# Performance work log

Hardware: AMD Instinct MI355X
Metric: run time of the kernel (lower is better)

The kernel has to match this reference:

```python
import jax, jax.numpy as jnp
import numpy as np

V, E, H, K = 50000, 256, 256, 16   # vocab, embed_dim, bi_lstm_hidden, n_tags (E must equal H)
HD = H // 2                        # per-direction hidden
B, NSEG, S = 32, 8, 128            # batch, segments, segment size
T = NSEG * S


def _lstm_dir(x, mask, Wih, Whh, b, h0, c0, reverse):
    """Masked (packed-equivalent) unidirectional LSTM. x:[T,B,E], mask:[T,B]."""
    def step(carry, inp):
        h, c = carry
        xt, mt = inp
        g = xt @ Wih.T + h @ Whh.T + b
        i, f, gg, o = jnp.split(g, 4, axis=-1)  # torch gate order i,f,g,o
        cn = jax.nn.sigmoid(f) * c + jax.nn.sigmoid(i) * jnp.tanh(gg)
        hn = jax.nn.sigmoid(o) * jnp.tanh(cn)
        m = mt[:, None]
        return (jnp.where(m, hn, h), jnp.where(m, cn, c)), jnp.where(m, hn, 0.0)
    (hT, cT), out = jax.lax.scan(step, (h0, c0), (x, mask), reverse=reverse)
    return out, (hT, cT)


def _bilstm(x, lengths, pf, pb, init=None):
    """pack_padded_sequence-equivalent BiLSTM. x:[T,B,E], lengths:[B]."""
    Tt, Bb = x.shape[0], x.shape[1]
    mask = jnp.arange(Tt)[:, None] < lengths[None, :]
    z = jnp.zeros((Bb, HD), x.dtype)
    h0f, c0f, h0b, c0b = init if init is not None else (z, z, z, z)
    of, (hf, cf) = _lstm_dir(x, mask, pf[0], pf[1], pf[2], h0f, c0f, False)
    ob, (hb, cb) = _lstm_dir(x, mask, pb[0], pb[1], pb[2], h0b, c0b, True)
    return jnp.concatenate([of, ob], -1), (hf, cf, hb, cb)


def _viterbi(emission, mask, start, trans, end):
    """torchcrf-style masked Viterbi decode. emission:[T,B,K], mask:[T,B]."""
    score = start[None, :] + emission[0]  # [B,K]
    def step(sc, inp):
        em, m = inp
        allsc = sc[:, :, None] + trans[None, :, :] + em[:, None, :]  # [B,K,K]
        best = jnp.max(allsc, axis=1)
        idx = jnp.argmax(allsc, axis=1).astype(jnp.int32)
        return jnp.where(m[:, None], best, sc), idx
    final, hist = jax.lax.scan(step, score, (emission[1:], mask[1:]))
    final = final + end[None, :]
    best_score = jnp.max(final, axis=-1)                 # [B]
    last = jnp.argmax(final, axis=-1).astype(jnp.int32)  # [B]
    def back(cur, inp):
        h, m = inp  # h:[B,K] backpointers at step t, m = mask[t+1]
        prev = jnp.take_along_axis(h, cur[:, None], axis=1)[:, 0]
        cur = jnp.where(m, prev, cur)
        return cur, cur
    _, tags_rev = jax.lax.scan(back, last, (hist, mask[1:]), reverse=True)
    tags = jnp.concatenate([tags_rev, last[None]], axis=0)  # [T,B]
    return tags, best_score


def _forward(texts, lengths, emb_table, Wih_f, Whh_f, bih_f, bhh_f,
             Wih_b, Whh_b, bih_b, bhh_b, Wlin, blin,
             crf_start, crf_trans, crf_end):
    pf = (Wih_f, Whh_f, bih_f + bhh_f)
    pb = (Wih_b, Whh_b, bih_b + bhh_b)
    emb = emb_table[texts]                      # [B,NSEG,S,E]
    x = jnp.transpose(emb, (1, 2, 0, 3))        # [NSEG,S,B,E]
    lens_seg = lengths.T                        # [NSEG,B]
    # pass 1: independent BiLSTM per segment (zero init state)
    outs, hids = jax.vmap(lambda xs, ls: _bilstm(xs, ls, pf, pb))(x, lens_seg)
    # positions >= per-segment max length are the raw embeddings (torch.cat with pad_text)
    maxlen = jnp.max(lens_seg, axis=1)          # [NSEG]
    over = jnp.arange(S)[None, :, None] >= maxlen[:, None, None]  # [NSEG,S,1]
    outs = jnp.where(over[..., None], x, outs)  # relies on E == 2*HD == H
    lstm1 = outs.reshape(NSEG * S, B, H)        # torch.cat(outputs, dim=0) -> [T,B,H]
    # get_text_lengths: per sample, valid tokens of all segments first, then pad tokens
    t_idx = jnp.arange(T)
    seg, pos = t_idx // S, t_idx % S
    valid = pos[None, :] < lengths[:, seg]                 # [B,T]
    key2 = jnp.where(valid, t_idx[None, :], t_idx[None, :] + T)
    perm = jnp.argsort(key2, axis=1)                       # [B,T] stable reorder
    lstm1_bt = jnp.transpose(lstm1, (1, 0, 2))             # [B,T,H]
    lstm2_in = jnp.transpose(
        jnp.take_along_axis(lstm1_bt, perm[..., None], axis=1), (1, 0, 2))  # [T,B,H]
    new_len = jnp.sum(lengths, axis=1)                     # [B]
    # pass 2: same LSTM weights, init state = final hidden of LAST segment (self.hidden)
    hf, cf, hb, cb = hids
    init = (hf[-1], cf[-1], hb[-1], cb[-1])
    lstm2_out, _ = _bilstm(lstm2_in, new_len, pf, pb, init)
    emission = lstm2_out @ Wlin.T + blin[None, None, :]    # [T,B,K]
    mask = jnp.arange(T)[:, None] < new_len[None, :]       # [T,B]
    return _viterbi(emission, mask, crf_start, crf_trans, crf_end)


def setup_inputs() -> dict:
    key = jax.random.key(0)
    ks = jax.random.split(key, 16)
    def u(k, shape, n):
        s = 1.0 / np.sqrt(n)
        return jax.random.uniform(k, shape, jnp.float32, -s, s)
    return {
        "texts": jax.random.randint(ks[0], (B, NSEG, S), 0, V).astype(jnp.int32),
        "lengths": jax.random.randint(ks[1], (B, NSEG), 1, S + 1).astype(jnp.int32),
        "emb_table": jax.random.normal(ks[2], (V, E), jnp.float32),
        "Wih_f": u(ks[3], (4 * HD, E), HD), "Whh_f": u(ks[4], (4 * HD, HD), HD),
        "bih_f": u(ks[5], (4 * HD,), HD), "bhh_f": u(ks[6], (4 * HD,), HD),
        "Wih_b": u(ks[7], (4 * HD, E), HD), "Whh_b": u(ks[8], (4 * HD, HD), HD),
        "bih_b": u(ks[9], (4 * HD,), HD), "bhh_b": u(ks[10], (4 * HD,), HD),
        "Wlin": u(ks[11], (K, H), H), "blin": u(ks[12], (K,), H),
        "crf_start": jax.random.uniform(ks[13], (K,), jnp.float32, -0.1, 0.1),
        "crf_trans": jax.random.uniform(ks[14], (K, K), jnp.float32, -0.1, 0.1),
        "crf_end": jax.random.uniform(ks[15], (K,), jnp.float32, -0.1, 0.1),
    }


def reference(texts, lengths, emb_table, Wih_f, Whh_f, bih_f, bhh_f,
              Wih_b, Whh_b, bih_b, bhh_b, Wlin, blin,
              crf_start, crf_trans, crf_end):
    # returns (tags [T,B] int32 padded with last tag beyond each length, viterbi score [B])
    return _forward(texts, lengths, emb_table, Wih_f, Whh_f, bih_f, bhh_f,
                    Wih_b, Whh_b, bih_b, bhh_b, Wlin, blin,
                    crf_start, crf_trans, crf_end)
```

## Files before the change

kernel.cpp:

```cpp
#include <hip/hip_runtime.h>
#include <cstdint>
#include <cstddef>


#define B_    32
#define NSEG_ 8
#define S_    128
#define T_    1024
#define E_    256
#define HD_   128
#define G_    512
#define K_    16
#define KS_   8

#define PIN4(v) asm volatile("" : "+v"((v).x), "+v"((v).y), "+v"((v).z), "+v"((v).w))

#define BAR_LDS() do {                                        \
    asm volatile("s_waitcnt lgkmcnt(0)" ::: "memory");        \
    __builtin_amdgcn_s_barrier();                             \
    __builtin_amdgcn_sched_barrier(0);                        \
} while (0)

__global__ void prep_kernel(const int* __restrict__ lengths,
                            int* __restrict__ seg_off, int* __restrict__ new_len,
                            const float* __restrict__ bih_f, const float* __restrict__ bhh_f,
                            const float* __restrict__ bih_b, const float* __restrict__ bhh_b,
                            float* __restrict__ bias1,
                            const float* __restrict__ Wih_f, const float* __restrict__ Wih_b,
                            float* __restrict__ WT1)
{
    int gtid = blockIdx.x * blockDim.x + threadIdx.x;
    if (gtid < B_) {
        int acc = 0;
        for (int s = 0; s < NSEG_; s++) { seg_off[gtid*NSEG_ + s] = acc; acc += lengths[gtid*NSEG_ + s]; }
        new_len[gtid] = acc;
    }
    if (gtid < 1024) {
        int n = gtid, dir = n >> 9, j = (n >> 2) & 127, g = n & 3;
        int row = g*128 + j;
        bias1[n] = dir ? (bih_b[row] + bhh_b[row]) : (bih_f[row] + bhh_f[row]);
    }
    for (int e = gtid; e < 256*1024; e += gridDim.x * blockDim.x) {
        int k = e >> 10, n = e & 1023;
        int dir = n >> 9, j = (n >> 2) & 127, g = n & 3;
        int row = g*128 + j;
        WT1[e] = dir ? Wih_b[row*E_ + k] : Wih_f[row*E_ + k];
    }
}

template <int MODE>
__global__ void __launch_bounds__(256, 4)
proj_kernel(const int* __restrict__ texts, const float* __restrict__ emb,
            const float* __restrict__ WT1, const float* __restrict__ bias1,
            const float* __restrict__ lstm_packed, float* __restrict__ xproj,
            const int* __restrict__ seg_off, const int* __restrict__ new_len)
{
    int b  = blockIdx.z;
    int nl = new_len[b];
    int p0 = blockIdx.x * 32;
    if (p0 >= nl) return;
    int j0 = blockIdx.y * 256;

    __shared__ __align__(16) float As[32][256];
    __shared__ const float* rowp[32];
    int tid = threadIdx.x;
    if (tid < 32) {
        int p = p0 + tid;
        const float* r = emb;
        if (p < nl) {
            if (MODE == 0) {
                int sg = 0;
                #pragma unroll
                for (int q = 1; q < NSEG_; q++) if (seg_off[b*NSEG_ + q] <= p) sg = q;
                int t   = p - seg_off[b*NSEG_ + sg];
                int tok = texts[(b*NSEG_ + sg)*S_ + t];
                r = emb + (size_t)tok * E_;
            } else {
                r = lstm_packed + ((size_t)b*T_ + p) * 256;
            }
        }
        rowp[tid] = r;
    }
    __syncthreads();
    #pragma unroll 4
    for (int i = 0; i < 32; i++) As[i][tid] = rowp[i][tid];
    __syncthreads();

    int pg = tid >> 6;
    int jg = tid & 63;
    int j  = j0 + jg*4;
    float acc[8][4];
    #pragma unroll
    for (int i = 0; i < 8; i++) { acc[i][0]=0.f; acc[i][1]=0.f; acc[i][2]=0.f; acc[i][3]=0.f; }

    const float* wbase = WT1 + j;
    for (int k = 0; k < 256; k += 4) {
        float4 w0 = *(const float4*)(wbase + (size_t)(k+0)*1024);
        float4 w1 = *(const float4*)(wbase + (size_t)(k+1)*1024);
        float4 w2 = *(const float4*)(wbase + (size_t)(k+2)*1024);
        float4 w3 = *(const float4*)(wbase + (size_t)(k+3)*1024);
        #pragma unroll
        for (int i = 0; i < 8; i++) {
            float4 a = *(const float4*)&As[pg*8 + i][k];
            acc[i][0] = fmaf(a.w, w3.x, fmaf(a.z, w2.x, fmaf(a.y, w1.x, fmaf(a.x, w0.x, acc[i][0]))));
            acc[i][1] = fmaf(a.w, w3.y, fmaf(a.z, w2.y, fmaf(a.y, w1.y, fmaf(a.x, w0.y, acc[i][1]))));
            acc[i][2] = fmaf(a.w, w3.z, fmaf(a.z, w2.z, fmaf(a.y, w1.z, fmaf(a.x, w0.z, acc[i][2]))));
            acc[i][3] = fmaf(a.w, w3.w, fmaf(a.z, w2.w, fmaf(a.y, w1.w, fmaf(a.x, w0.w, acc[i][3]))));
        }
    }
    float4 bs = *(const float4*)(bias1 + j);
    #pragma unroll
    for (int i = 0; i < 8; i++) {
        int p = p0 + pg*8 + i;
        if (p < nl) {
            float4 r;
            r.x = acc[i][0] + bs.x; r.y = acc[i][1] + bs.y;
            r.z = acc[i][2] + bs.z; r.w = acc[i][3] + bs.w;
            *(float4*)(xproj + (((size_t)b*T_ + p) << 10) + j) = r;
        }
    }
}

__device__ __forceinline__ float sig_f(float x) { return 1.0f / (1.0f + __expf(-x)); }
__device__ __forceinline__ float tanh_f(float x) {
    float xc = fminf(fmaxf(x, -15.0f), 15.0f);
    float e  = __expf(-2.0f * xc);
    return (1.0f - e) / (1.0f + e);
}

__device__ __forceinline__ void lstm_chain(
    const float* __restrict__ Whh,
    const float* __restrict__ xp,
    float* __restrict__ outp,
    int p_base, int len, int dir, int rev,
    const float* __restrict__ h0, const float* __restrict__ c0,
    float* __restrict__ hT, float* __restrict__ cT)
{
    __shared__ __align__(16) float  h_sh[HD_];
    __shared__ __align__(16) float4 psum[4*HD_];
    int t = threadIdx.x;
    int j = t & 127, q = t >> 7;

    float4 w[4][8];
    #pragma unroll
    for (int g = 0; g < 4; g++) {
        const float4* wr = (const float4*)(Whh + (size_t)(j + 128*g) * HD_ + 32*q);
        #pragma unroll
        for (int i = 0; i < 8; i++) { w[g][i] = wr[i]; PIN4(w[g][i]); }
    }

    float c_reg = 0.0f;
    if (t < HD_) {
        h_sh[t] = h0 ? h0[t] : 0.0f;
        c_reg   = c0 ? c0[t] : 0.0f;
    }
    __syncthreads();

    const float4* xcol4 = (const float4*)(xp + (size_t)dir * G_) + j;
    const int     oco   = dir * HD_ + j;

    float4 xv[KS_];
    float  hbuf[KS_];

    for (int gs = 0; gs < len; gs += KS_) {
        if (t < HD_) {
            if (gs > 0) {
                #pragma unroll
                for (int u = 0; u < KS_; u++) {
                    int s = gs - KS_ + u;
                    int p = p_base + (rev ? (len - 1 - s) : s);
                    outp[(size_t)p * 256 + oco] = hbuf[u];
                }
            }
            #pragma unroll
            for (int u = 0; u < KS_; u++) {
                int s = gs + u;
                if (s < len) {
                    int p = p_base + (rev ? (len - 1 - s) : s);
                    xv[u] = xcol4[(size_t)p << 8];
                }
            }
        }
        #pragma unroll
        for (int u = 0; u < KS_; u++) {
            if (gs + u < len) {
                const float4* hv = (const float4*)h_sh + q * 8;
                float4 a0 = make_float4(0.f,0.f,0.f,0.f);
                float4 a1 = a0, a2 = a0, a3 = a0;
                #pragma unroll
                for (int i = 0; i < 8; i++) {
                    float4 h4 = hv[i];
                    a0.x = fmaf(h4.x, w[0][i].x, a0.x); a0.y = fmaf(h4.y, w[0][i].y, a0.y);
                    a0.z = fmaf(h4.z, w[0][i].z, a0.z); a0.w = fmaf(h4.w, w[0][i].w, a0.w);
                    a1.x = fmaf(h4.x, w[1][i].x, a1.x); a1.y = fmaf(h4.y, w[1][i].y, a1.y);
                    a1.z = fmaf(h4.z, w[1][i].z, a1.z); a1.w = fmaf(h4.w, w[1][i].w, a1.w);
                    a2.x = fmaf(h4.x, w[2][i].x, a2.x); a2.y = fmaf(h4.y, w[2][i].y, a2.y);
                    a2.z = fmaf(h4.z, w[2][i].z, a2.z); a2.w = fmaf(h4.w, w[2][i].w, a2.w);
                    a3.x = fmaf(h4.x, w[3][i].x, a3.x); a3.y = fmaf(h4.y, w[3][i].y, a3.y);
                    a3.z = fmaf(h4.z, w[3][i].z, a3.z); a3.w = fmaf(h4.w, w[3][i].w, a3.w);
                }
                psum[q*128 + j] = make_float4((a0.x+a0.y)+(a0.z+a0.w),
                                              (a1.x+a1.y)+(a1.z+a1.w),
                                              (a2.x+a2.y)+(a2.z+a2.w),
                                              (a3.x+a3.y)+(a3.z+a3.w));
                BAR_LDS();
                if (t < HD_) {
                    float4 p0 = psum[j], p1 = psum[128 + j], p2 = psum[256 + j], p3 = psum[384 + j];
                    float gi = xv[u].x + ((p0.x + p1.x) + (p2.x + p3.x));
                    float gf = xv[u].y + ((p0.y + p1.y) + (p2.y + p3.y));
                    float gg = xv[u].z + ((p0.z + p1.z) + (p2.z + p3.z));
                    float go = xv[u].w + ((p0.w + p1.w) + (p2.w + p3.w));
                    float cn = sig_f(gf) * c_reg + sig_f(gi) * tanh_f(gg);
                    c_reg = cn;
                    float hn = sig_f(go) * tanh_f(cn);
                    h_sh[j] = hn;
                    hbuf[u] = hn;
                }
                BAR_LDS();
            }
        }
    }
    if (t < HD_ && len > 0) {
        int gs = ((len - 1) / KS_) * KS_;
        #pragma unroll
        for (int u = 0; u < KS_; u++) {
            int s = gs + u;
            if (s < len) {
                int p = p_base + (rev ? (len - 1 - s) : s);
                outp[(size_t)p * 256 + oco] = hbuf[u];
            }
        }
    }
    if (hT != nullptr && t < HD_) { hT[t] = h_sh[t]; cT[t] = c_reg; }
}

__global__ void __launch_bounds__(512, 1)
lstm1_kernel(const int* __restrict__ lengths, const int* __restrict__ seg_off,
             const float* __restrict__ Whh_f, const float* __restrict__ Whh_b,
             const float* __restrict__ xproj, float* __restrict__ lstm_packed,
             float* __restrict__ hinit, float* __restrict__ cinit)
{
    int cid = blockIdx.x;
    int b = cid >> 4, seg = (cid >> 1) & 7, dir = cid & 1;
    int len = lengths[b*NSEG_ + seg];
    int pb  = seg_off[b*NSEG_ + seg];
    const float* Whh = dir ? Whh_b : Whh_f;
    float* hT = nullptr; float* cT = nullptr;
    if (seg == NSEG_ - 1) {
        hT = hinit + (dir*B_ + b)*HD_;
        cT = cinit + (dir*B_ + b)*HD_;
    }
    lstm_chain(Whh, xproj + ((size_t)b << 20), lstm_packed + (size_t)b*T_*256,
               pb, len, dir, dir, nullptr, nullptr, hT, cT);
}

__global__ void __launch_bounds__(512, 1)
lstm2_kernel(const int* __restrict__ new_len,
             const float* __restrict__ Whh_f, const float* __restrict__ Whh_b,
             const float* __restrict__ xproj, float* __restrict__ lstm_packed,
             const float* __restrict__ hinit, const float* __restrict__ cinit)
{
    int cid = blockIdx.x;
    int b = cid >> 1, dir = cid & 1;
    int len = new_len[b];
    const float* Whh = dir ? Whh_b : Whh_f;
    lstm_chain(Whh, xproj + ((size_t)b << 20), lstm_packed + (size_t)b*T_*256,
               0, len, dir, dir,
               hinit + (dir*B_ + b)*HD_, cinit + (dir*B_ + b)*HD_,
               nullptr, nullptr);
}

__global__ void __launch_bounds__(256)
emission_kernel(const float* __restrict__ lstm_packed, const float* __restrict__ Wlin,
                const float* __restrict__ blin, float* __restrict__ emis,
                const int* __restrict__ new_len)
{
    int b  = blockIdx.y;
    int nl = new_len[b];
    int p0 = blockIdx.x * 16;
    if (p0 >= nl) return;
    int pl = threadIdx.x >> 4, s = threadIdx.x & 15;
    int p  = p0 + pl;
    const float4* xr = (const float4*)(lstm_packed + ((size_t)b*T_ + p) * 256);
    const float4* wr = (const float4*)(Wlin + (size_t)s * 256);
    float ax = 0.f, ay = 0.f, az = 0.f, aw = 0.f;
    #pragma unroll
    for (int i = 0; i < 64; i++) {
        float4 a = xr[i]; float4 ww = wr[i];
        ax = fmaf(a.x, ww.x, ax); ay = fmaf(a.y, ww.y, ay);
        az = fmaf(a.z, ww.z, az); aw = fmaf(a.w, ww.w, aw);
    }
    if (p < nl) emis[((size_t)b*T_ + p)*K_ + s] = (ax + ay) + (az + aw) + blin[s];
}

__global__ void __launch_bounds__(64)
viterbi_kernel(const float* __restrict__ emis, const float* __restrict__ start,
               const float* __restrict__ trans, const float* __restrict__ endv,
               const int* __restrict__ new_len, float* __restrict__ out)
{
    int b    = blockIdx.x;
    int nl   = new_len[b];
    int lane = threadIdx.x;
    int s    = lane & 15, q4 = lane >> 4;

    __shared__ unsigned char hist[T_ * K_];
    __shared__ unsigned char tagb[T_];

    float tr[4];
    #pragma unroll
    for (int jj = 0; jj < 4; jj++) tr[jj] = trans[(q4*4 + jj)*K_ + s];

    const float* em = emis + (size_t)b * T_ * K_;
    float sc = start[s] + em[s];

    for (int p = 1; p < nl; p++) {
        float e = em[p*K_ + s];
        float m = -3.4e38f; int a = 0;
        #pragma unroll
        for (int jj = 0; jj < 4; jj++) {
            int q   = q4*4 + jj;
            float sq = __shfl(sc, q, 16);
            float v  = sq + tr[jj];
            if (v > m) { m = v; a = q; }
        }
        #pragma unroll
        for (int d = 16; d < 64; d <<= 1) {
            float mo = __shfl_xor(m, d);
            int   ao = __shfl_xor(a, d);
            if (mo > m || (mo == m && ao < a)) { m = mo; a = ao; }
        }
        sc = m + e;
        if (lane < K_) hist[p*K_ + s] = (unsigned char)a;
    }

    float m = sc + endv[s]; int a = s;
    #pragma unroll
    for (int d = 1; d < 16; d <<= 1) {
        float mo = __shfl_xor(m, d);
        int   ao = __shfl_xor(a, d);
        if (mo > m || (mo == m && ao < a)) { m = mo; a = ao; }
    }
    int last = a;
    if (lane == 0) out[T_*B_ + b] = m;
    __syncthreads();

    for (int i = lane; i < T_; i += 64) tagb[i] = (unsigned char)last;
    __syncthreads();
    if (lane == 0) {
        int cur = last;
        for (int j = nl - 2; j >= 0; j--) {
            cur = hist[(j+1)*K_ + cur];
            tagb[j] = (unsigned char)cur;
        }
    }
    __syncthreads();
    for (int i = lane; i < T_; i += 64) out[(size_t)i*B_ + b] = (float)tagb[i];
}

extern "C" void kernel_launch(void* const* d_in, const int* in_sizes, int n_in,
                              void* d_out, int out_size, void* d_ws, size_t ws_size,
                              hipStream_t stream)
{
    (void)in_sizes; (void)n_in; (void)out_size; (void)ws_size;
    const int*   texts   = (const int*)  d_in[0];
    const int*   lengths = (const int*)  d_in[1];
    const float* emb     = (const float*)d_in[2];
    const float* Wih_f   = (const float*)d_in[3];
    const float* Whh_f   = (const float*)d_in[4];
    const float* bih_f   = (const float*)d_in[5];
    const float* bhh_f   = (const float*)d_in[6];
    const float* Wih_b   = (const float*)d_in[7];
    const float* Whh_b   = (const float*)d_in[8];
    const float* bih_b   = (const float*)d_in[9];
    const float* bhh_b   = (const float*)d_in[10];
    const float* Wlin    = (const float*)d_in[11];
    const float* blin    = (const float*)d_in[12];
    const float* c_start = (const float*)d_in[13];
    const float* c_trans = (const float*)d_in[14];
    const float* c_end   = (const float*)d_in[15];
    float* out = (float*)d_out;

    char* w = (char*)d_ws;
    int*   seg_off     = (int*)(w);
    int*   new_len     = (int*)(w + 1024);
    float* bias1       = (float*)(w + 4096);
    float* WT1         = (float*)(w + 8192);
    float* hinit       = (float*)(w + 8192 + 1048576);
    float* cinit       = hinit + 8192;
    float* lstm_packed = cinit + 8192;
    float* xproj       = lstm_packed + (size_t)B_*T_*256;
    float* emis        = xproj + ((size_t)B_ << 20);

    prep_kernel<<<128, 256, 0, stream>>>(lengths, seg_off, new_len,
                                         bih_f, bhh_f, bih_b, bhh_b, bias1,
                                         Wih_f, Wih_b, WT1);
    proj_kernel<0><<<dim3(32, 4, B_), 256, 0, stream>>>(texts, emb, WT1, bias1,
                                                        lstm_packed, xproj, seg_off, new_len);
    lstm1_kernel<<<512, 512, 0, stream>>>(lengths, seg_off, Whh_f, Whh_b,
                                          xproj, lstm_packed, hinit, cinit);
    proj_kernel<1><<<dim3(32, 4, B_), 256, 0, stream>>>(texts, emb, WT1, bias1,
                                                        lstm_packed, xproj, seg_off, new_len);
    lstm2_kernel<<<64, 512, 0, stream>>>(new_len, Whh_f, Whh_b,
                                         xproj, lstm_packed, hinit, cinit);
    emission_kernel<<<dim3(64, B_), 256, 0, stream>>>(lstm_packed, Wlin, blin, emis, new_len);
    viterbi_kernel<<<B_, 64, 0, stream>>>(emis, c_start, c_trans, c_end, new_len, out);
}
```

Measured before the change: 1.587 ms.

## Interleave two LSTM chains per block and pair batches by length

Each LSTM block now processes two independent recurrences sharing the same Whh registers, alternating one chain's matvec with the other's gate update so barrier and transcendental latency overlap. lstm1 pairs adjacent segments, and lstm2 pairs longest-with-shortest batches via a length sort computed in prep_kernel. This halves block counts and double-buffers x-projection prefetch. It trades extra LDS and per-pair load imbalance for fewer idle cycles per step.

New measurement: 1.744 ms. +9.9%, slower.

```diff
diff --git a/kernel.cpp b/kernel.cpp
--- a/kernel.cpp
+++ b/kernel.cpp
@@ -11,7 +11,6 @@
 #define HD_   128
 #define G_    512
 #define K_    16
-#define KS_   8
 
 #define PIN4(v) asm volatile("" : "+v"((v).x), "+v"((v).y), "+v"((v).z), "+v"((v).w))
 
@@ -23,12 +22,15 @@
 
 __global__ void prep_kernel(const int* __restrict__ lengths,
                             int* __restrict__ seg_off, int* __restrict__ new_len,
+                            int* __restrict__ pairs,
                             const float* __restrict__ bih_f, const float* __restrict__ bhh_f,
                             const float* __restrict__ bih_b, const float* __restrict__ bhh_b,
                             float* __restrict__ bias1,
                             const float* __restrict__ Wih_f, const float* __restrict__ Wih_b,
                             float* __restrict__ WT1)
 {
+    __shared__ int s_len[B_];
+    __shared__ int s_sorted[B_];
     int gtid = blockIdx.x * blockDim.x + threadIdx.x;
     if (gtid < B_) {
         int acc = 0;
@@ -39,6 +41,25 @@
         int n = gtid, dir = n >> 9, j = (n >> 2) & 127, g = n & 3;
         int row = g*128 + j;
         bias1[n] = dir ? (bih_b[row] + bhh_b[row]) : (bih_f[row] + bhh_f[row]);
+    }
+    if (blockIdx.x == 0) {
+        int t = threadIdx.x;
+        if (t < B_) {
+            int acc = 0;
+            for (int s = 0; s < NSEG_; s++) acc += lengths[t*NSEG_ + s];
+            s_len[t] = acc;
+        }
+        __syncthreads();
+        if (t < B_) {
+            int my = s_len[t], rank = 0;
+            for (int u = 0; u < B_; u++) {
+                int lu = s_len[u];
+                if (lu < my || (lu == my && u < t)) rank++;
+            }
+            s_sorted[rank] = t;
+        }
+        __syncthreads();
+        if (t < B_/2) { pairs[2*t] = s_sorted[t]; pairs[2*t+1] = s_sorted[B_-1-t]; }
     }
     for (int e = gtid; e < 256*1024; e += gridDim.x * blockDim.x) {
         int k = e >> 10, n = e & 1023;
@@ -128,16 +149,60 @@
     return (1.0f - e) / (1.0f + e);
 }
 
-__device__ __forceinline__ void lstm_chain(
+__device__ __forceinline__ void matvec_step(const float4 (&w)[4][8],
+                                            const float* __restrict__ h_sh,
+                                            float4* __restrict__ psum,
+                                            int j, int q)
+{
+    const float4* hv = (const float4*)h_sh + q * 8;
+    float4 a0 = make_float4(0.f,0.f,0.f,0.f);
+    float4 a1 = a0, a2 = a0, a3 = a0;
+    #pragma unroll
+    for (int i = 0; i < 8; i++) {
+        float4 h4 = hv[i];
+        a0.x = fmaf(h4.x, w[0][i].x, a0.x); a0.y = fmaf(h4.y, w[0][i].y, a0.y);
+        a0.z = fmaf(h4.z, w[0][i].z, a0.z); a0.w = fmaf(h4.w, w[0][i].w, a0.w);
+        a1.x = fmaf(h4.x, w[1][i].x, a1.x); a1.y = fmaf(h4.y, w[1][i].y, a1.y);
+        a1.z = fmaf(h4.z, w[1][i].z, a1.z); a1.w = fmaf(h4.w, w[1][i].w, a1.w);
+        a2.x = fmaf(h4.x, w[2][i].x, a2.x); a2.y = fmaf(h4.y, w[2][i].y, a2.y);
+        a2.z = fmaf(h4.z, w[2][i].z, a2.z); a2.w = fmaf(h4.w, w[2][i].w, a2.w);
+        a3.x = fmaf(h4.x, w[3][i].x, a3.x); a3.y = fmaf(h4.y, w[3][i].y, a3.y);
+        a3.z = fmaf(h4.z, w[3][i].z, a3.z); a3.w = fmaf(h4.w, w[3][i].w, a3.w);
+    }
+    psum[q*128 + j] = make_float4((a0.x+a0.y)+(a0.z+a0.w),
+                                  (a1.x+a1.y)+(a1.z+a1.w),
+                                  (a2.x+a2.y)+(a2.z+a2.w),
+                                  (a3.x+a3.y)+(a3.z+a3.w));
+}
+
+__device__ __forceinline__ float reduce_step(const float4* __restrict__ ps,
+                                             float4 xv, float& c_reg,
+                                             float* __restrict__ h_sh, int j)
+{
+    float4 p0 = ps[j], p1 = ps[128 + j], p2 = ps[256 + j], p3 = ps[384 + j];
+    float gi = xv.x + ((p0.x + p1.x) + (p2.x + p3.x));
+    float gf = xv.y + ((p0.y + p1.y) + (p2.y + p3.y));
+    float gg = xv.z + ((p0.z + p1.z) + (p2.z + p3.z));
+    float go = xv.w + ((p0.w + p1.w) + (p2.w + p3.w));
+    float cn = sig_f(gf) * c_reg + sig_f(gi) * tanh_f(gg);
+    c_reg = cn;
+    float hn = sig_f(go) * tanh_f(cn);
+    h_sh[j] = hn;
+    return hn;
+}
+
+__device__ __forceinline__ void lstm_fused(
     const float* __restrict__ Whh,
-    const float* __restrict__ xp,
-    float* __restrict__ outp,
-    int p_base, int len, int dir, int rev,
-    const float* __restrict__ h0, const float* __restrict__ c0,
-    float* __restrict__ hT, float* __restrict__ cT)
-{
-    __shared__ __align__(16) float  h_sh[HD_];
-    __shared__ __align__(16) float4 psum[4*HD_];
+    const float* __restrict__ xpA, const float* __restrict__ xpB,
+    float* __restrict__ outA, float* __restrict__ outB,
+    int pbA, int lenA, int pbB, int lenB, int dir,
+    const float* __restrict__ h0A, const float* __restrict__ c0A,
+    const float* __restrict__ h0B, const float* __restrict__ c0B,
+    float* __restrict__ hTA, float* __restrict__ cTA,
+    float* __restrict__ hTB, float* __restrict__ cTB)
+{
+    __shared__ __align__(16) float  h_A[HD_], h_B[HD_];
+    __shared__ __align__(16) float4 psA[4*HD_], psB[4*HD_];
     int t = threadIdx.x;
     int j = t & 127, q = t >> 7;
 
@@ -149,89 +214,58 @@
         for (int i = 0; i < 8; i++) { w[g][i] = wr[i]; PIN4(w[g][i]); }
     }
 
-    float c_reg = 0.0f;
+    float cA = 0.0f, cB = 0.0f;
     if (t < HD_) {
-        h_sh[t] = h0 ? h0[t] : 0.0f;
-        c_reg   = c0 ? c0[t] : 0.0f;
-    }
-    __syncthreads();
-
-    const float4* xcol4 = (const float4*)(xp + (size_t)dir * G_) + j;
-    const int     oco   = dir * HD_ + j;
-
-    float4 xv[KS_];
-    float  hbuf[KS_];
-
-    for (int gs = 0; gs < len; gs += KS_) {
-        if (t < HD_) {
-            if (gs > 0) {
-                #pragma unroll
-                for (int u = 0; u < KS_; u++) {
-                    int s = gs - KS_ + u;
-                    int p = p_base + (rev ? (len - 1 - s) : s);
-                    outp[(size_t)p * 256 + oco] = hbuf[u];
-                }
+        h_A[t] = h0A ? h0A[t] : 0.0f;  cA = c0A ? c0A[t] : 0.0f;
+        h_B[t] = h0B ? h0B[t] : 0.0f;  cB = c0B ? c0B[t] : 0.0f;
+    }
+
+    const float4* xcA = (const float4*)(xpA + (size_t)dir * G_) + j;
+    const float4* xcB = (const float4*)(xpB + (size_t)dir * G_) + j;
+    const int rev = dir;
+    const int oco = dir * HD_ + j;
+
+    auto pA = [&](int s) { return pbA + (rev ? (lenA - 1 - s) : s); };
+    auto pB = [&](int s) { return pbB + (rev ? (lenB - 1 - s) : s); };
+
+    float4 zero4 = make_float4(0.f,0.f,0.f,0.f);
+    float4 xvAc = zero4, xvAn = zero4, xvBc = zero4, xvBn = zero4;
+    if (t < HD_) {
+        if (0 < lenA) xvAc = xcA[(size_t)pA(0) << 8];
+        if (1 < lenA) xvAn = xcA[(size_t)pA(1) << 8];
+        if (0 < lenB) xvBc = xcB[(size_t)pB(0) << 8];
+        if (1 < lenB) xvBn = xcB[(size_t)pB(1) << 8];
+    }
+    __syncthreads();
+
+    int maxlen = lenA > lenB ? lenA : lenB;
+    for (int it = 0; it <= maxlen; it++) {
+        if (it >= 1 && it - 1 < lenB) {
+            if (t < HD_) {
+                float4 xu = xvBc; xvBc = xvBn;
+                if (it + 1 < lenB) xvBn = xcB[(size_t)pB(it + 1) << 8];
+                float hn = reduce_step(psB, xu, cB, h_B, j);
+                outB[(size_t)pB(it - 1) * 256 + oco] = hn;
             }
-            #pragma unroll
-            for (int u = 0; u < KS_; u++) {
-                int s = gs + u;
-                if (s < len) {
-                    int p = p_base + (rev ? (len - 1 - s) : s);
-                    xv[u] = xcol4[(size_t)p << 8];
-                }
+        }
+        if (it < lenA) matvec_step(w, h_A, psA, j, q);
+        BAR_LDS();
+        if (it < lenA) {
+            if (t < HD_) {
+                float4 xu = xvAc; xvAc = xvAn;
+                if (it + 2 < lenA) xvAn = xcA[(size_t)pA(it + 2) << 8];
+                float hn = reduce_step(psA, xu, cA, h_A, j);
+                outA[(size_t)pA(it) * 256 + oco] = hn;
             }
         }
-        #pragma unroll
-        for (int u = 0; u < KS_; u++) {
-            if (gs + u < len) {
-                const float4* hv = (const float4*)h_sh + q * 8;
-                float4 a0 = make_float4(0.f,0.f,0.f,0.f);
-                float4 a1 = a0, a2 = a0, a3 = a0;
-                #pragma unroll
-                for (int i = 0; i < 8; i++) {
-                    float4 h4 = hv[i];
-                    a0.x = fmaf(h4.x, w[0][i].x, a0.x); a0.y = fmaf(h4.y, w[0][i].y, a0.y);
-                    a0.z = fmaf(h4.z, w[0][i].z, a0.z); a0.w = fmaf(h4.w, w[0][i].w, a0.w);
-                    a1.x = fmaf(h4.x, w[1][i].x, a1.x); a1.y = fmaf(h4.y, w[1][i].y, a1.y);
-                    a1.z = fmaf(h4.z, w[1][i].z, a1.z); a1.w = fmaf(h4.w, w[1][i].w, a1.w);
-                    a2.x = fmaf(h4.x, w[2][i].x, a2.x); a2.y = fmaf(h4.y, w[2][i].y, a2.y);
-                    a2.z = fmaf(h4.z, w[2][i].z, a2.z); a2.w = fmaf(h4.w, w[2][i].w, a2.w);
-                    a3.x = fmaf(h4.x, w[3][i].x, a3.x); a3.y = fmaf(h4.y, w[3][i].y, a3.y);
-                    a3.z = fmaf(h4.z, w[3][i].z, a3.z); a3.w = fmaf(h4.w, w[3][i].w, a3.w);
-                }
-                psum[q*128 + j] = make_float4((a0.x+a0.y)+(a0.z+a0.w),
-                                              (a1.x+a1.y)+(a1.z+a1.w),
-                                              (a2.x+a2.y)+(a2.z+a2.w),
-                                              (a3.x+a3.y)+(a3.z+a3.w));
-                BAR_LDS();
-                if (t < HD_) {
-                    float4 p0 = psum[j], p1 = psum[128 + j], p2 = psum[256 + j], p3 = psum[384 + j];
-                    float gi = xv[u].x + ((p0.x + p1.x) + (p2.x + p3.x));
-                    float gf = xv[u].y + ((p0.y + p1.y) + (p2.y + p3.y));
-                    float gg = xv[u].z + ((p0.z + p1.z) + (p2.z + p3.z));
-                    float go = xv[u].w + ((p0.w + p1.w) + (p2.w + p3.w));
-                    float cn = sig_f(gf) * c_reg + sig_f(gi) * tanh_f(gg);
-                    c_reg = cn;
-                    float hn = sig_f(go) * tanh_f(cn);
-                    h_sh[j] = hn;
-                    hbuf[u] = hn;
-                }
-                BAR_LDS();
-            }
-        }
-    }
-    if (t < HD_ && len > 0) {
-        int gs = ((len - 1) / KS_) * KS_;
-        #pragma unroll
-        for (int u = 0; u < KS_; u++) {
-            int s = gs + u;
-            if (s < len) {
-                int p = p_base + (rev ? (len - 1 - s) : s);
-                outp[(size_t)p * 256 + oco] = hbuf[u];
-            }
-        }
-    }
-    if (hT != nullptr && t < HD_) { hT[t] = h_sh[t]; cT[t] = c_reg; }
+        if (it < lenB) matvec_step(w, h_B, psB, j, q);
+        BAR_LDS();
+    }
+
+    if (t < HD_) {
+        if (hTA != nullptr) { hTA[t] = h_A[t]; cTA[t] = cA; }
+        if (hTB != nullptr) { hTB[t] = h_B[t]; cTB[t] = cB; }
+    }
 }
 
 __global__ void __launch_bounds__(512, 1)
@@ -241,33 +275,41 @@
              float* __restrict__ hinit, float* __restrict__ cinit)
 {
     int cid = blockIdx.x;
-    int b = cid >> 4, seg = (cid >> 1) & 7, dir = cid & 1;
-    int len = lengths[b*NSEG_ + seg];
-    int pb  = seg_off[b*NSEG_ + seg];
+    int b = cid >> 3, sp = (cid >> 1) & 3, dir = cid & 1;
+    int segA = 2*sp, segB = 2*sp + 1;
+    int lenA = lengths[b*NSEG_ + segA], lenB = lengths[b*NSEG_ + segB];
+    int pbA  = seg_off[b*NSEG_ + segA], pbB  = seg_off[b*NSEG_ + segB];
     const float* Whh = dir ? Whh_b : Whh_f;
     float* hT = nullptr; float* cT = nullptr;
-    if (seg == NSEG_ - 1) {
+    if (sp == 3) {
         hT = hinit + (dir*B_ + b)*HD_;
         cT = cinit + (dir*B_ + b)*HD_;
     }
-    lstm_chain(Whh, xproj + ((size_t)b << 20), lstm_packed + (size_t)b*T_*256,
-               pb, len, dir, dir, nullptr, nullptr, hT, cT);
+    const float* xp = xproj + ((size_t)b << 20);
+    float* outp = lstm_packed + (size_t)b*T_*256;
+    lstm_fused(Whh, xp, xp, outp, outp, pbA, lenA, pbB, lenB, dir,
+               nullptr, nullptr, nullptr, nullptr,
+               nullptr, nullptr, hT, cT);
 }
 
 __global__ void __launch_bounds__(512, 1)
-lstm2_kernel(const int* __restrict__ new_len,
+lstm2_kernel(const int* __restrict__ new_len, const int* __restrict__ pairs,
              const float* __restrict__ Whh_f, const float* __restrict__ Whh_b,
              const float* __restrict__ xproj, float* __restrict__ lstm_packed,
              const float* __restrict__ hinit, const float* __restrict__ cinit)
 {
     int cid = blockIdx.x;
-    int b = cid >> 1, dir = cid & 1;
-    int len = new_len[b];
+    int dir = cid >> 4, pi = cid & 15;
+    int bA = pairs[2*pi], bB = pairs[2*pi + 1];
+    int lenA = new_len[bA], lenB = new_len[bB];
     const float* Whh = dir ? Whh_b : Whh_f;
-    lstm_chain(Whh, xproj + ((size_t)b << 20), lstm_packed + (size_t)b*T_*256,
-               0, len, dir, dir,
-               hinit + (dir*B_ + b)*HD_, cinit + (dir*B_ + b)*HD_,
-               nullptr, nullptr);
+    lstm_fused(Whh,
+               xproj + ((size_t)bA << 20), xproj + ((size_t)bB << 20),
+               lstm_packed + (size_t)bA*T_*256, lstm_packed + (size_t)bB*T_*256,
+               0, lenA, 0, lenB, dir,
+               hinit + (dir*B_ + bA)*HD_, cinit + (dir*B_ + bA)*HD_,
+               hinit + (dir*B_ + bB)*HD_, cinit + (dir*B_ + bB)*HD_,
+               nullptr, nullptr, nullptr, nullptr);
 }
 
 __global__ void __launch_bounds__(256)
@@ -383,6 +425,7 @@
     char* w = (char*)d_ws;
     int*   seg_off     = (int*)(w);
     int*   new_len     = (int*)(w + 1024);
+    int*   pairs       = (int*)(w + 2048);
     float* bias1       = (float*)(w + 4096);
     float* WT1         = (float*)(w + 8192);
     float* hinit       = (float*)(w + 8192 + 1048576);
@@ -391,16 +434,16 @@
     float* xproj       = lstm_packed + (size_t)B_*T_*256;
     float* emis        = xproj + ((size_t)B_ << 20);
 
-    prep_kernel<<<128, 256, 0, stream>>>(lengths, seg_off, new_len,
+    prep_kernel<<<128, 256, 0, stream>>>(lengths, seg_off, new_len, pairs,
                                          bih_f, bhh_f, bih_b, bhh_b, bias1,
                                          Wih_f, Wih_b, WT1);
     proj_kernel<0><<<dim3(32, 4, B_), 256, 0, stream>>>(texts, emb, WT1, bias1,
                                                         lstm_packed, xproj, seg_off, new_len);
-    lstm1_kernel<<<512, 512, 0, stream>>>(lengths, seg_off, Whh_f, Whh_b,
+    lstm1_kernel<<<256, 512, 0, stream>>>(lengths, seg_off, Whh_f, Whh_b,
                                           xproj, lstm_packed, hinit, cinit);
     proj_kernel<1><<<dim3(32, 4, B_), 256, 0, stream>>>(texts, emb, WT1, bias1,
                                                         lstm_packed, xproj, seg_off, new_len);
-    lstm2_kernel<<<64, 512, 0, stream>>>(new_len, Whh_f, Whh_b,
+    lstm2_kernel<<<32, 512, 0, stream>>>(new_len, pairs, Whh_f, Whh_b,
                                          xproj, lstm_packed, hinit, cinit);
     emission_kernel<<<dim3(64, B_), 256, 0, stream>>>(lstm_packed, Wlin, blin, emis, new_len);
     viterbi_kernel<<<B_, 64, 0, stream>>>(emis, c_start, c_trans, c_end, new_len, out);
```

## Reduce LSTM gate partials with wave shuffles and double-buffer hidden state

Applied to the files above, without the earlier changes.

Each hidden unit's four-way split of the recurrent dot product now sits in four adjacent lanes, so the partial sums are combined with xor shuffles instead of a psum LDS array. That removes one of the two block barriers per timestep. The hidden state is double-buffered in padded LDS so a single barrier per step is enough. The input projection is prefetched two steps ahead instead of in batches of eight, and launch bounds ask for two blocks per CU. All 512 threads now run the gate math redundantly, and the occupancy hint may increase register pressure given the 128 pinned weight registers.

After: 1.799 ms. +13.3%, slower.

```diff
diff --git a/kernel.cpp b/kernel.cpp
--- a/kernel.cpp
+++ b/kernel.cpp
@@ -11,7 +11,6 @@
 #define HD_   128
 #define G_    512
 #define K_    16
-#define KS_   8
 
 #define PIN4(v) asm volatile("" : "+v"((v).x), "+v"((v).y), "+v"((v).z), "+v"((v).w))
 
@@ -136,10 +135,9 @@
     const float* __restrict__ h0, const float* __restrict__ c0,
     float* __restrict__ hT, float* __restrict__ cT)
 {
-    __shared__ __align__(16) float  h_sh[HD_];
-    __shared__ __align__(16) float4 psum[4*HD_];
+    __shared__ __align__(16) float h_sh[2][4*36];
     int t = threadIdx.x;
-    int j = t & 127, q = t >> 7;
+    int j = t >> 2, q = t & 3;
 
     float4 w[4][8];
     #pragma unroll
@@ -149,92 +147,68 @@
         for (int i = 0; i < 8; i++) { w[g][i] = wr[i]; PIN4(w[g][i]); }
     }
 
-    float c_reg = 0.0f;
-    if (t < HD_) {
-        h_sh[t] = h0 ? h0[t] : 0.0f;
-        c_reg   = c0 ? c0[t] : 0.0f;
-    }
-    __syncthreads();
-
-    const float4* xcol4 = (const float4*)(xp + (size_t)dir * G_) + j;
-    const int     oco   = dir * HD_ + j;
-
-    float4 xv[KS_];
-    float  hbuf[KS_];
-
-    for (int gs = 0; gs < len; gs += KS_) {
-        if (t < HD_) {
-            if (gs > 0) {
-                #pragma unroll
-                for (int u = 0; u < KS_; u++) {
-                    int s = gs - KS_ + u;
-                    int p = p_base + (rev ? (len - 1 - s) : s);
-                    outp[(size_t)p * 256 + oco] = hbuf[u];
-                }
-            }
-            #pragma unroll
-            for (int u = 0; u < KS_; u++) {
-                int s = gs + u;
-                if (s < len) {
-                    int p = p_base + (rev ? (len - 1 - s) : s);
-                    xv[u] = xcol4[(size_t)p << 8];
-                }
-            }
-        }
-        #pragma unroll
-        for (int u = 0; u < KS_; u++) {
-            if (gs + u < len) {
-                const float4* hv = (const float4*)h_sh + q * 8;
-                float4 a0 = make_float4(0.f,0.f,0.f,0.f);
-                float4 a1 = a0, a2 = a0, a3 = a0;
-                #pragma unroll
-                for (int i = 0; i < 8; i++) {
-                    float4 h4 = hv[i];
-                    a0.x = fmaf(h4.x, w[0][i].x, a0.x); a0.y = fmaf(h4.y, w[0][i].y, a0.y);
-                    a0.z = fmaf(h4.z, w[0][i].z, a0.z); a0.w = fmaf(h4.w, w[0][i].w, a0.w);
-                    a1.x = fmaf(h4.x, w[1][i].x, a1.x); a1.y = fmaf(h4.y, w[1][i].y, a1.y);
-                    a1.z = fmaf(h4.z, w[1][i].z, a1.z); a1.w = fmaf(h4.w, w[1][i].w, a1.w);
-                    a2.x = fmaf(h4.x, w[2][i].x, a2.x); a2.y = fmaf(h4.y, w[2][i].y, a2.y);
-                    a2.z = fmaf(h4.z, w[2][i].z, a2.z); a2.w = fmaf(h4.w, w[2][i].w, a2.w);
-                    a3.x = fmaf(h4.x, w[3][i].x, a3.x); a3.y = fmaf(h4.y, w[3][i].y, a3.y);
-                    a3.z = fmaf(h4.z, w[3][i].z, a3.z); a3.w = fmaf(h4.w, w[3][i].w, a3.w);
-                }
-                psum[q*128 + j] = make_float4((a0.x+a0.y)+(a0.z+a0.w),
-                                              (a1.x+a1.y)+(a1.z+a1.w),
-                                              (a2.x+a2.y)+(a2.z+a2.w),
-                                              (a3.x+a3.y)+(a3.z+a3.w));
-                BAR_LDS();
-                if (t < HD_) {
-                    float4 p0 = psum[j], p1 = psum[128 + j], p2 = psum[256 + j], p3 = psum[384 + j];
-                    float gi = xv[u].x + ((p0.x + p1.x) + (p2.x + p3.x));
-                    float gf = xv[u].y + ((p0.y + p1.y) + (p2.y + p3.y));
-                    float gg = xv[u].z + ((p0.z + p1.z) + (p2.z + p3.z));
-                    float go = xv[u].w + ((p0.w + p1.w) + (p2.w + p3.w));
-                    float cn = sig_f(gf) * c_reg + sig_f(gi) * tanh_f(gg);
-                    c_reg = cn;
-                    float hn = sig_f(go) * tanh_f(cn);
-                    h_sh[j] = hn;
-                    hbuf[u] = hn;
-                }
-                BAR_LDS();
-            }
-        }
-    }
-    if (t < HD_ && len > 0) {
-        int gs = ((len - 1) / KS_) * KS_;
-        #pragma unroll
-        for (int u = 0; u < KS_; u++) {
-            int s = gs + u;
-            if (s < len) {
-                int p = p_base + (rev ? (len - 1 - s) : s);
-                outp[(size_t)p * 256 + oco] = hbuf[u];
-            }
-        }
-    }
-    if (hT != nullptr && t < HD_) { hT[t] = h_sh[t]; cT[t] = c_reg; }
-}
-
-__global__ void __launch_bounds__(512, 1)
+    float c_reg = c0 ? c0[j] : 0.0f;
+    if (q == 0) h_sh[0][(j >> 5)*36 + (j & 31)] = h0 ? h0[j] : 0.0f;
+
+    const float4* xc  = (const float4*)(xp + (size_t)dir * G_) + j;
+    const int     oco = dir * HD_ + j;
+
+    float4 xvc = make_float4(0.f,0.f,0.f,0.f), xvn = xvc;
+    if (len > 0) xvc = xc[(size_t)(p_base + (rev ? len-1 : 0)) << 8];
+    if (len > 1) xvn = xc[(size_t)(p_base + (rev ? len-2 : 1)) << 8];
+    __syncthreads();
+
+    for (int it = 0; it < len; it++) {
+        int p_out = p_base + (rev ? (len-1-it) : it);
+        float4 xu = xvc; xvc = xvn;
+        if (it + 2 < len) xvn = xc[(size_t)(p_base + (rev ? (len-3-it) : (it+2))) << 8];
+
+        const float4* hv = (const float4*)(h_sh[it & 1] + q*36);
+        float4 a0 = make_float4(0.f,0.f,0.f,0.f);
+        float4 a1 = a0, a2 = a0, a3 = a0;
+        #pragma unroll
+        for (int i = 0; i < 8; i++) {
+            float4 h4 = hv[i];
+            a0.x = fmaf(h4.x, w[0][i].x, a0.x); a0.y = fmaf(h4.y, w[0][i].y, a0.y);
+            a0.z = fmaf(h4.z, w[0][i].z, a0.z); a0.w = fmaf(h4.w, w[0][i].w, a0.w);
+            a1.x = fmaf(h4.x, w[1][i].x, a1.x); a1.y = fmaf(h4.y, w[1][i].y, a1.y);
+            a1.z = fmaf(h4.z, w[1][i].z, a1.z); a1.w = fmaf(h4.w, w[1][i].w, a1.w);
+            a2.x = fmaf(h4.x, w[2][i].x, a2.x); a2.y = fmaf(h4.y, w[2][i].y, a2.y);
+            a2.z = fmaf(h4.z, w[2][i].z, a2.z); a2.w = fmaf(h4.w, w[2][i].w, a2.w);
+            a3.x = fmaf(h4.x, w[3][i].x, a3.x); a3.y = fmaf(h4.y, w[3][i].y, a3.y);
+            a3.z = fmaf(h4.z, w[3][i].z, a3.z); a3.w = fmaf(h4.w, w[3][i].w, a3.w);
+        }
+        float4 part;
+        part.x = (a0.x+a0.y)+(a0.z+a0.w);
+        part.y = (a1.x+a1.y)+(a1.z+a1.w);
+        part.z = (a2.x+a2.y)+(a2.z+a2.w);
+        part.w = (a3.x+a3.y)+(a3.z+a3.w);
+        part.x += __shfl_xor(part.x, 1); part.y += __shfl_xor(part.y, 1);
+        part.z += __shfl_xor(part.z, 1); part.w += __shfl_xor(part.w, 1);
+        part.x += __shfl_xor(part.x, 2); part.y += __shfl_xor(part.y, 2);
+        part.z += __shfl_xor(part.z, 2); part.w += __shfl_xor(part.w, 2);
+
+        float gi = xu.x + part.x;
+        float gf = xu.y + part.y;
+        float gg = xu.z + part.z;
+        float go = xu.w + part.w;
+        float cn = sig_f(gf) * c_reg + sig_f(gi) * tanh_f(gg);
+        c_reg = cn;
+        float hn = sig_f(go) * tanh_f(cn);
+        if (q == 0) {
+            h_sh[(it+1) & 1][(j >> 5)*36 + (j & 31)] = hn;
+            outp[(size_t)p_out * 256 + oco] = hn;
+        }
+        BAR_LDS();
+    }
+
+    if (q == 0 && hT != nullptr) {
+        hT[j] = h_sh[len & 1][(j >> 5)*36 + (j & 31)];
+        cT[j] = c_reg;
+    }
+}
+
+__global__ void __launch_bounds__(512, 2)
 lstm1_kernel(const int* __restrict__ lengths, const int* __restrict__ seg_off,
              const float* __restrict__ Whh_f, const float* __restrict__ Whh_b,
              const float* __restrict__ xproj, float* __restrict__ lstm_packed,
@@ -254,7 +228,7 @@
                pb, len, dir, dir, nullptr, nullptr, hT, cT);
 }
 
-__global__ void __launch_bounds__(512, 1)
+__global__ void __launch_bounds__(512, 2)
 lstm2_kernel(const int* __restrict__ new_len,
              const float* __restrict__ Whh_f, const float* __restrict__ Whh_b,
              const float* __restrict__ xproj, float* __restrict__ lstm_packed,
```

## Schedule lstm1 segments longest-first and widen projection tile to 8 columns

Applied to the files above, without the earlier changes.

prep_kernel now ranks the 256 (batch, segment) pairs by length in descending order, and lstm1 blocks take their segment from that order. Long recurrent chains therefore start first, which should reduce the tail of the kernel when 512 single-occupancy blocks run on the available CUs. Separately, the projection GEMM has each thread compute 8 output columns instead of 4, halving grid.y so each A tile in LDS is reused over twice as many columns. This costs more registers, and the launch bound drops from 4 to 2 blocks per CU.

Measured after the change: 1.562 ms. Within noise of the previous version (-1.6%).

```diff
diff --git a/kernel.cpp b/kernel.cpp
--- a/kernel.cpp
+++ b/kernel.cpp
@@ -23,12 +23,15 @@
 
 __global__ void prep_kernel(const int* __restrict__ lengths,
                             int* __restrict__ seg_off, int* __restrict__ new_len,
+                            int* __restrict__ order1,
                             const float* __restrict__ bih_f, const float* __restrict__ bhh_f,
                             const float* __restrict__ bih_b, const float* __restrict__ bhh_b,
                             float* __restrict__ bias1,
                             const float* __restrict__ Wih_f, const float* __restrict__ Wih_b,
                             float* __restrict__ WT1)
 {
+    __shared__ int s_len[256];
+    __shared__ int s_ord[256];
     int gtid = blockIdx.x * blockDim.x + threadIdx.x;
     if (gtid < B_) {
         int acc = 0;
@@ -40,6 +43,19 @@
         int row = g*128 + j;
         bias1[n] = dir ? (bih_b[row] + bhh_b[row]) : (bih_f[row] + bhh_f[row]);
     }
+    if (blockIdx.x == 0) {
+        int t = threadIdx.x;
+        s_len[t] = lengths[t];
+        __syncthreads();
+        int my = s_len[t], rank = 0;
+        for (int u = 0; u < 256; u++) {
+            int lu = s_len[u];
+            if (lu > my || (lu == my && u < t)) rank++;
+        }
+        s_ord[rank] = t;
+        __syncthreads();
+        order1[t] = s_ord[t];
+    }
     for (int e = gtid; e < 256*1024; e += gridDim.x * blockDim.x) {
         int k = e >> 10, n = e & 1023;
         int dir = n >> 9, j = (n >> 2) & 127, g = n & 3;
@@ -49,7 +65,7 @@
 }
 
 template <int MODE>
-__global__ void __launch_bounds__(256, 4)
+__global__ void __launch_bounds__(256, 2)
 proj_kernel(const int* __restrict__ texts, const float* __restrict__ emb,
             const float* __restrict__ WT1, const float* __restrict__ bias1,
             const float* __restrict__ lstm_packed, float* __restrict__ xproj,
@@ -59,7 +75,7 @@
     int nl = new_len[b];
     int p0 = blockIdx.x * 32;
     if (p0 >= nl) return;
-    int j0 = blockIdx.y * 256;
+    int j0 = blockIdx.y * 512;
 
     __shared__ __align__(16) float As[32][256];
     __shared__ const float* rowp[32];
@@ -88,35 +104,50 @@
 
     int pg = tid >> 6;
     int jg = tid & 63;
-    int j  = j0 + jg*4;
-    float acc[8][4];
-    #pragma unroll
-    for (int i = 0; i < 8; i++) { acc[i][0]=0.f; acc[i][1]=0.f; acc[i][2]=0.f; acc[i][3]=0.f; }
+    int j  = j0 + jg*8;
+    float acc[8][8];
+    #pragma unroll
+    for (int i = 0; i < 8; i++)
+        #pragma unroll
+        for (int c = 0; c < 8; c++) acc[i][c] = 0.f;
 
     const float* wbase = WT1 + j;
     for (int k = 0; k < 256; k += 4) {
-        float4 w0 = *(const float4*)(wbase + (size_t)(k+0)*1024);
-        float4 w1 = *(const float4*)(wbase + (size_t)(k+1)*1024);
-        float4 w2 = *(const float4*)(wbase + (size_t)(k+2)*1024);
-        float4 w3 = *(const float4*)(wbase + (size_t)(k+3)*1024);
+        float4 w00 = *(const float4*)(wbase + (size_t)(k+0)*1024);
+        float4 w01 = *(const float4*)(wbase + (size_t)(k+0)*1024 + 4);
+        float4 w10 = *(const float4*)(wbase + (size_t)(k+1)*1024);
+        float4 w11 = *(const float4*)(wbase + (size_t)(k+1)*1024 + 4);
+        float4 w20 = *(const float4*)(wbase + (size_t)(k+2)*1024);
+        float4 w21 = *(const float4*)(wbase + (size_t)(k+2)*1024 + 4);
+        float4 w30 = *(const float4*)(wbase + (size_t)(k+3)*1024);
+        float4 w31 = *(const float4*)(wbase + (size_t)(k+3)*1024 + 4);
         #pragma unroll
         for (int i = 0; i < 8; i++) {
             float4 a = *(const float4*)&As[pg*8 + i][k];
-            acc[i][0] = fmaf(a.w, w3.x, fmaf(a.z, w2.x, fmaf(a.y, w1.x, fmaf(a.x, w0.x, acc[i][0]))));
-            acc[i][1] = fmaf(a.w, w3.y, fmaf(a.z, w2.y, fmaf(a.y, w1.y, fmaf(a.x, w0.y, acc[i][1]))));
-            acc[i][2] = fmaf(a.w, w3.z, fmaf(a.z, w2.z, fmaf(a.y, w1.z, fmaf(a.x, w0.z, acc[i][2]))));
-            acc[i][3] = fmaf(a.w, w3.w, fmaf(a.z, w2.w, fmaf(a.y, w1.w, fmaf(a.x, w0.w, acc[i][3]))));
-        }
-    }
-    float4 bs = *(const float4*)(bias1 + j);
+            acc[i][0] = fmaf(a.w, w30.x, fmaf(a.z, w20.x, fmaf(a.y, w10.x, fmaf(a.x, w00.x, acc[i][0]))));
+            acc[i][1] = fmaf(a.w, w30.y, fmaf(a.z, w20.y, fmaf(a.y, w10.y, fmaf(a.x, w00.y, acc[i][1]))));
+            acc[i][2] = fmaf(a.w, w30.z, fmaf(a.z, w20.z, fmaf(a.y, w10.z, fmaf(a.x, w00.z, acc[i][2]))));
+            acc[i][3] = fmaf(a.w, w30.w, fmaf(a.z, w20.w, fmaf(a.y, w10.w, fmaf(a.x, w00.w, acc[i][3]))));
+            acc[i][4] = fmaf(a.w, w31.x, fmaf(a.z, w21.x, fmaf(a.y, w11.x, fmaf(a.x, w01.x, acc[i][4]))));
+            acc[i][5] = fmaf(a.w, w31.y, fmaf(a.z, w21.y, fmaf(a.y, w11.y, fmaf(a.x, w01.y, acc[i][5]))));
+            acc[i][6] = fmaf(a.w, w31.z, fmaf(a.z, w21.z, fmaf(a.y, w11.z, fmaf(a.x, w01.z, acc[i][6]))));
+            acc[i][7] = fmaf(a.w, w31.w, fmaf(a.z, w21.w, fmaf(a.y, w11.w, fmaf(a.x, w01.w, acc[i][7]))));
+        }
+    }
+    float4 bs0 = *(const float4*)(bias1 + j);
+    float4 bs1 = *(const float4*)(bias1 + j + 4);
     #pragma unroll
     for (int i = 0; i < 8; i++) {
         int p = p0 + pg*8 + i;
         if (p < nl) {
-            float4 r;
-            r.x = acc[i][0] + bs.x; r.y = acc[i][1] + bs.y;
-            r.z = acc[i][2] + bs.z; r.w = acc[i][3] + bs.w;
-            *(float4*)(xproj + (((size_t)b*T_ + p) << 10) + j) = r;
+            float4 r0, r1;
+            r0.x = acc[i][0] + bs0.x; r0.y = acc[i][1] + bs0.y;
+            r0.z = acc[i][2] + bs0.z; r0.w = acc[i][3] + bs0.w;
+            r1.x = acc[i][4] + bs1.x; r1.y = acc[i][5] + bs1.y;
+            r1.z = acc[i][6] + bs1.z; r1.w = acc[i][7] + bs1.w;
+            float* dst = xproj + (((size_t)b*T_ + p) << 10) + j;
+            *(float4*)dst       = r0;
+            *(float4*)(dst + 4) = r1;
         }
     }
 }
@@ -236,12 +267,14 @@
 
 __global__ void __launch_bounds__(512, 1)
 lstm1_kernel(const int* __restrict__ lengths, const int* __restrict__ seg_off,
+             const int* __restrict__ order1,
              const float* __restrict__ Whh_f, const float* __restrict__ Whh_b,
              const float* __restrict__ xproj, float* __restrict__ lstm_packed,
              float* __restrict__ hinit, float* __restrict__ cinit)
 {
     int cid = blockIdx.x;
-    int b = cid >> 4, seg = (cid >> 1) & 7, dir = cid & 1;
+    int pr  = order1[cid >> 1];
+    int b = pr >> 3, seg = pr & 7, dir = cid & 1;
     int len = lengths[b*NSEG_ + seg];
     int pb  = seg_off[b*NSEG_ + seg];
     const float* Whh = dir ? Whh_b : Whh_f;
@@ -383,6 +416,7 @@
     char* w = (char*)d_ws;
     int*   seg_off     = (int*)(w);
     int*   new_len     = (int*)(w + 1024);
+    int*   order1      = (int*)(w + 2048);
     float* bias1       = (float*)(w + 4096);
     float* WT1         = (float*)(w + 8192);
     float* hinit       = (float*)(w + 8192 + 1048576);
@@ -391,14 +425,14 @@
     float* xproj       = lstm_packed + (size_t)B_*T_*256;
     float* emis        = xproj + ((size_t)B_ << 20);
 
-    prep_kernel<<<128, 256, 0, stream>>>(lengths, seg_off, new_len,
+    prep_kernel<<<128, 256, 0, stream>>>(lengths, seg_off, new_len, order1,
                                          bih_f, bhh_f, bih_b, bhh_b, bias1,
                                          Wih_f, Wih_b, WT1);
-    proj_kernel<0><<<dim3(32, 4, B_), 256, 0, stream>>>(texts, emb, WT1, bias1,
+    proj_kernel<0><<<dim3(32, 2, B_), 256, 0, stream>>>(texts, emb, WT1, bias1,
                                                         lstm_packed, xproj, seg_off, new_len);
-    lstm1_kernel<<<512, 512, 0, stream>>>(lengths, seg_off, Whh_f, Whh_b,
+    lstm1_kernel<<<512, 512, 0, stream>>>(lengths, seg_off, order1, Whh_f, Whh_b,
                                           xproj, lstm_packed, hinit, cinit);
-    proj_kernel<1><<<dim3(32, 4, B_), 256, 0, stream>>>(texts, emb, WT1, bias1,
+    proj_kernel<1><<<dim3(32, 2, B_), 256, 0, stream>>>(texts, emb, WT1, bias1,
                                                         lstm_packed, xproj, seg_off, new_len);
     lstm2_kernel<<<64, 512, 0, stream>>>(new_len, Whh_f, Whh_b,
                                          xproj, lstm_packed, hinit, cinit);
```
